# Performance work log

Hardware: AMD Instinct MI355X
Metric: run time of the kernel (lower is better)

Reference implementation:

```python
import jax, jax.numpy as jnp
import numpy as np

D_MODEL = 1024
N_HEADS = 16
D_K = D_MODEL // N_HEADS


def setup_inputs() -> dict:
    key = jax.random.key(0)
    ks = jax.random.split(key, 9)
    s = 1.0 / np.sqrt(D_MODEL)
    def lin(kw, kb):
        W = jax.random.uniform(kw, (D_MODEL, D_MODEL), jnp.float32, -s, s)
        b = jax.random.uniform(kb, (D_MODEL,), jnp.float32, -s, s)
        return W, b
    wq, bq = lin(ks[0], ks[1])
    wk, bk = lin(ks[2], ks[3])
    wv, bv = lin(ks[4], ks[5])
    wo, bo = lin(ks[6], ks[7])
    x = jax.random.normal(ks[8], (2, 2048, D_MODEL), jnp.float32)
    return {"x": x, "wq": wq, "bq": bq, "wk": wk, "bk": bk,
            "wv": wv, "bv": bv, "wo": wo, "bo": bo}


def reference(x, wq, bq, wk, bk, wv, bv, wo, bo):
    B, S, D = x.shape
    scale = 1.0 / np.sqrt(D_K)
    # projections (torch Linear: y = x W^T + b); W stored as [in,out] here
    q = x @ wq + bq
    k = x @ wk + bk
    v = x @ wv + bv
    # [B, H, S, d_k]
    q = q.reshape(B, S, N_HEADS, D_K).transpose(0, 2, 1, 3)
    k = k.reshape(B, S, N_HEADS, D_K).transpose(0, 2, 1, 3)
    v = v.reshape(B, S, N_HEADS, D_K).transpose(0, 2, 1, 3)
    scores = jnp.einsum('bhqd,bhkd->bhqk', q, k) * scale
    attn = jax.nn.softmax(scores, axis=-1)
    out = jnp.einsum('bhqk,bhkd->bhqd', attn, v)
    out = out.transpose(0, 2, 1, 3).reshape(B, S, D)
    return out @ wo + bo
```

## Files before the change

### kernel.cpp

```cpp
#include <hip/hip_runtime.h>
#include <hip/hip_bf16.h>
#include <math.h>

typedef __bf16 bf16x8 __attribute__((ext_vector_type(8)));
typedef unsigned short u16x8 __attribute__((ext_vector_type(8)));
typedef unsigned short u16x4 __attribute__((ext_vector_type(4)));
typedef float f32x4 __attribute__((ext_vector_type(4)));
typedef unsigned int u32x4 __attribute__((ext_vector_type(4)));
typedef unsigned int u32x2 __attribute__((ext_vector_type(2)));
typedef unsigned short u16;

__device__ __forceinline__ u16 f2bf(float f) {
    unsigned int x = __float_as_uint(f);
    x += 0x7fffu + ((x >> 16) & 1u);
    return (u16)(x >> 16);
}
__device__ __forceinline__ void glds16(const void* g, void* l) {
    __builtin_amdgcn_global_load_lds(
        (const __attribute__((address_space(1))) void*)g,
        (__attribute__((address_space(3))) void*)l, 16, 0, 0);
}
__device__ __forceinline__ void swap_half(unsigned& a, unsigned& b) {
    u32x2 t = __builtin_amdgcn_permlane32_swap(a, b, false, false);
    t = __builtin_amdgcn_permlane16_swap(t[0], t[1], false, false);
    a = t[0]; b = t[1];
}

__global__ __launch_bounds__(256) void prep(const float* __restrict__ W0, const float* __restrict__ W1,
                                            const float* __restrict__ W2, const float* __restrict__ W3,
                                            const float* __restrict__ X,
                                            u16* __restrict__ Wt, u16* __restrict__ Xb) {
    int z = blockIdx.z;
    if (z >= 4) {
        int row = (z - 4) * 1024 + blockIdx.y * 32 + blockIdx.x;
        const float* src = X + (size_t)row * 1024 + threadIdx.x * 4;
        f32x4 v = *(const f32x4*)src;
        u16x4 o; o[0] = f2bf(v[0]); o[1] = f2bf(v[1]); o[2] = f2bf(v[2]); o[3] = f2bf(v[3]);
        *(u16x4*)&Xb[(size_t)row * 1024 + threadIdx.x * 4] = o;
        return;
    }
    __shared__ float T[32][33];
    const float* W = (z == 0) ? W0 : ((z == 1) ? W1 : ((z == 2) ? W2 : W3));
    u16* dst = Wt + (size_t)z * 1024 * 1024;
    int k0 = blockIdx.y * 32, n0 = blockIdx.x * 32;
    int x = threadIdx.x & 31, y0 = threadIdx.x >> 5;
#pragma unroll
    for (int i = 0; i < 4; i++) {
        int y = y0 + i * 8;
        T[y][x] = W[(size_t)(k0 + y) * 1024 + n0 + x];
    }
    __syncthreads();
#pragma unroll
    for (int i = 0; i < 4; i++) {
        int y = y0 + i * 8;
        dst[(size_t)(n0 + y) * 1024 + k0 + x] = f2bf(T[x][y]);
    }
}

template <bool OF32, bool VSPLIT>
__global__ __launch_bounds__(256) void gemm(
    const u16* __restrict__ Bt,
    const float* __restrict__ b0, const float* __restrict__ b1, const float* __restrict__ b2,
    const u16* __restrict__ A, void* __restrict__ Cptr, u16* __restrict__ Vt, int Ntot)
{
    __shared__ __align__(16) u16 As[128 * 32];
    __shared__ __align__(16) u16 Bs[128 * 32];
    int tid = threadIdx.x;
    int lane = tid & 63, l15 = lane & 15, quad = lane >> 4;
    int wid = tid >> 6, wm = wid >> 1, wn = wid & 1;
    int m0 = blockIdx.y * 128, n0 = blockIdx.x * 128;
    int sel = n0 >> 10;
    const float* bias = (sel == 0) ? b0 : ((sel == 1) ? b1 : b2);

    f32x4 acc[4][4];
#pragma unroll
    for (int i = 0; i < 4; i++)
#pragma unroll
        for (int j = 0; j < 4; j++) { f32x4 z = {0.f, 0.f, 0.f, 0.f}; acc[i][j] = z; }

    int rr = lane >> 2;
    int cc = (lane & 3) ^ ((rr >> 1) & 3);
    const u16* abase = A  + (size_t)m0 * 1024;
    const u16* bbase = Bt + (size_t)n0 * 1024;
    int fsw = (l15 >> 1) & 3;

    for (int k0 = 0; k0 < 1024; k0 += 32) {
#pragma unroll
        for (int inst = 0; inst < 2; inst++) {
            int r0 = wid * 32 + inst * 16;
            glds16(&abase[(size_t)(r0 + rr) * 1024 + k0 + cc * 8], &As[r0 * 32]);
            glds16(&bbase[(size_t)(r0 + rr) * 1024 + k0 + cc * 8], &Bs[r0 * 32]);
        }
        __syncthreads();
        bf16x8 af[4], bf[4];
#pragma unroll
        for (int mt = 0; mt < 4; mt++)
            af[mt] = *(const bf16x8*)&As[(wm * 64 + mt * 16 + l15) * 32 + ((quad ^ fsw) * 8)];
#pragma unroll
        for (int nt = 0; nt < 4; nt++)
            bf[nt] = *(const bf16x8*)&Bs[(wn * 64 + nt * 16 + l15) * 32 + ((quad ^ fsw) * 8)];
#pragma unroll
        for (int mt = 0; mt < 4; mt++)
#pragma unroll
            for (int nt = 0; nt < 4; nt++)
                acc[mt][nt] = __builtin_amdgcn_mfma_f32_16x16x32_bf16(af[mt], bf[nt], acc[mt][nt], 0, 0, 0);
        __syncthreads();
    }
    if (VSPLIT && sel == 2) {
        int b = m0 >> 11;
#pragma unroll
        for (int mt = 0; mt < 4; mt++) {
            int gr = m0 + wm * 64 + mt * 16 + quad * 4;
            int s = gr & 2047;
#pragma unroll
            for (int nt = 0; nt < 4; nt++) {
                int gcl = (n0 & 1023) + wn * 64 + nt * 16 + l15;
                float bb = bias[gcl];
                u16x4 pk;
#pragma unroll
                for (int r = 0; r < 4; r++) pk[r] = f2bf(acc[mt][nt][r] + bb);
                *(u16x4*)&Vt[(size_t)((b * 16 + (gcl >> 6)) * 64 + (gcl & 63)) * 2048 + s] = pk;
            }
        }
        return;
    }
#pragma unroll
    for (int mt = 0; mt < 4; mt++) {
        int gr = m0 + wm * 64 + mt * 16 + quad * 4;
#pragma unroll
        for (int nt = 0; nt < 4; nt++) {
            int gc = n0 + wn * 64 + nt * 16 + l15;
            float bb = bias[gc & 1023];
#pragma unroll
            for (int r = 0; r < 4; r++) {
                float v = acc[mt][nt][r] + bb;
                if (OF32) ((float*)Cptr)[(size_t)(gr + r) * Ntot + gc] = v;
                else      ((u16*)Cptr)[(size_t)(gr + r) * Ntot + gc] = f2bf(v);
            }
        }
    }
}

__global__ __launch_bounds__(256) void attn(const u16* __restrict__ QKV,
                                            const u16* __restrict__ Vt,
                                            u16* __restrict__ O)
{
    __shared__ __align__(16) u16 Ks[2][64 * 64];
    __shared__ __align__(16) u16 Vs[2][64 * 64];
    const int S = 2048, DQ = 3072;
    int tid = threadIdx.x, wid = tid >> 6, lane = tid & 63;
    int l15 = lane & 15, quad = lane >> 4;
    int qt = blockIdx.x, h = blockIdx.y, b = blockIdx.z;
    const u16* base = QKV + (size_t)b * S * DQ + h * 64;
    const u16* Kb = base + 1024;
    const u16* Vtb = Vt + (size_t)((b * 16 + h) * 64) * 2048;
    int q0 = qt * 64 + wid * 16;

    bf16x8 qf0 = *(const bf16x8*)&base[(size_t)(q0 + l15) * DQ + quad * 8];
    bf16x8 qf1 = *(const bf16x8*)&base[(size_t)(q0 + l15) * DQ + 32 + quad * 8];

    f32x4 oacc[4];
#pragma unroll
    for (int i = 0; i < 4; i++) { f32x4 z = {0.f, 0.f, 0.f, 0.f}; oacc[i] = z; }
    float psum = 0.f;
    const float ls = 0.125f * 1.44269504088896f;

    int rr = lane >> 3;
    int cc = (lane & 7) ^ rr;
    int fs7 = l15 & 7;

    auto stage = [&](int it, int bsel) {
        int kv0 = it << 6;
#pragma unroll
        for (int inst = 0; inst < 2; inst++) {
            int r0 = wid * 16 + inst * 8;
            glds16(&Kb[(size_t)(kv0 + r0 + rr) * DQ + cc * 8], &Ks[bsel][r0 * 64]);
            glds16(&Vtb[(size_t)(r0 + rr) * 2048 + kv0 + cc * 8], &Vs[bsel][r0 * 64]);
        }
    };

    stage(0, 0);
#pragma unroll 2
    for (int it = 0; it < 32; ++it) {
        int cur = it & 1;
        if (it < 31) {
            stage(it + 1, cur ^ 1);
            asm volatile("s_waitcnt vmcnt(4)\n\ts_barrier" ::: "memory");
        } else {
            asm volatile("s_waitcnt vmcnt(0)\n\ts_barrier" ::: "memory");
        }

        f32x4 sa[4];
#pragma unroll
        for (int t = 0; t < 4; t++) { f32x4 z = {0.f, 0.f, 0.f, 0.f}; sa[t] = z; }
#pragma unroll
        for (int t = 0; t < 4; t++) {
            bf16x8 kfa = *(const bf16x8*)&Ks[cur][(t * 16 + l15) * 64 + ((quad ^ fs7) * 8)];
            bf16x8 kfb = *(const bf16x8*)&Ks[cur][(t * 16 + l15) * 64 + (((quad + 4) ^ fs7) * 8)];
            sa[t] = __builtin_amdgcn_mfma_f32_16x16x32_bf16(kfa, qf0, sa[t], 0, 0, 0);
            sa[t] = __builtin_amdgcn_mfma_f32_16x16x32_bf16(kfb, qf1, sa[t], 0, 0, 0);
        }

        unsigned wpk[4][2];
#pragma unroll
        for (int t = 0; t < 4; t++) {
            float e0 = __builtin_amdgcn_exp2f(sa[t][0] * ls);
            float e1 = __builtin_amdgcn_exp2f(sa[t][1] * ls);
            float e2 = __builtin_amdgcn_exp2f(sa[t][2] * ls);
            float e3 = __builtin_amdgcn_exp2f(sa[t][3] * ls);
            psum += (e0 + e1) + (e2 + e3);
            asm("v_cvt_pk_bf16_f32 %0, %1, %2" : "=v"(wpk[t][0]) : "v"(e0), "v"(e1));
            asm("v_cvt_pk_bf16_f32 %0, %1, %2" : "=v"(wpk[t][1]) : "v"(e2), "v"(e3));
        }
        unsigned a0 = wpk[0][0], a2 = wpk[1][0]; swap_half(a0, a2);
        unsigned a1 = wpk[0][1], a3 = wpk[1][1]; swap_half(a1, a3);
        unsigned c0 = wpk[2][0], c2 = wpk[3][0]; swap_half(c0, c2);
        unsigned c1 = wpk[2][1], c3 = wpk[3][1]; swap_half(c1, c3);
        u32x4 pd0 = {a0, a1, a2, a3};
        u32x4 pd1 = {c0, c1, c2, c3};
        bf16x8 pf0 = *(bf16x8*)&pd0;
        bf16x8 pf1 = *(bf16x8*)&pd1;

#pragma unroll
        for (int dt = 0; dt < 4; dt++) {
            bf16x8 vfa = *(const bf16x8*)&Vs[cur][(dt * 16 + l15) * 64 + ((quad ^ fs7) * 8)];
            bf16x8 vfb = *(const bf16x8*)&Vs[cur][(dt * 16 + l15) * 64 + (((quad + 4) ^ fs7) * 8)];
            oacc[dt] = __builtin_amdgcn_mfma_f32_16x16x32_bf16(pf0, vfa, oacc[dt], 0, 0, 0);
            oacc[dt] = __builtin_amdgcn_mfma_f32_16x16x32_bf16(pf1, vfb, oacc[dt], 0, 0, 0);
        }
        asm volatile("s_barrier" ::: "memory");
    }

    psum += __shfl_xor(psum, 16);
    psum += __shfl_xor(psum, 32);
#pragma unroll
    for (int r = 0; r < 4; r++) {
        float inv = 1.0f / __shfl(psum, quad * 4 + r);
        size_t row = (size_t)(b * S + q0 + quad * 4 + r);
#pragma unroll
        for (int dt = 0; dt < 4; dt++)
            O[row * 1024 + h * 64 + dt * 16 + l15] = f2bf(oacc[dt][r] * inv);
    }
}

extern "C" void kernel_launch(void* const* d_in, const int* in_sizes, int n_in,
                              void* d_out, int out_size, void* d_ws, size_t ws_size,
                              hipStream_t stream) {
    const float* x  = (const float*)d_in[0];
    const float* wq = (const float*)d_in[1];
    const float* bq = (const float*)d_in[2];
    const float* wk = (const float*)d_in[3];
    const float* bk = (const float*)d_in[4];
    const float* wv = (const float*)d_in[5];
    const float* bv = (const float*)d_in[6];
    const float* wo = (const float*)d_in[7];
    const float* bo = (const float*)d_in[8];
    float* out = (float*)d_out;

    u16* qkv  = (u16*)d_ws;
    u16* obuf = qkv  + (size_t)4096 * 3072;
    u16* vt   = obuf + (size_t)4096 * 1024;
    u16* wt   = vt   + (size_t)2048 * 2048;
    u16* xb   = wt   + (size_t)4 * 1024 * 1024;

    dim3 tb(256);
    prep<<<dim3(32, 32, 8), tb, 0, stream>>>(wq, wk, wv, wo, x, wt, xb);
    gemm<false, true><<<dim3(24, 32), tb, 0, stream>>>(wt, bq, bk, bv, xb, qkv, vt, 3072);
    attn<<<dim3(32, 16, 2), tb, 0, stream>>>(qkv, vt, obuf);
    gemm<true, false><<<dim3(8, 32), tb, 0, stream>>>(wt + (size_t)3 * 1024 * 1024,
                                                      bo, bo, bo, obuf, out, (u16*)nullptr, 1024);
}
```

Before: 210.1 us.

## Process 32 query rows per wave in attention and fold softmax scale into Q

Each attention wave now handles two 16-row query tiles, so every K and V fragment read from LDS feeds twice as many MFMAs. The grid is halved to match. The softmax scale and log2(e) factor move into the QKV GEMM epilogue for the Q slice, which removes one multiply per score. The cost is more registers per thread (launch bounds set to 2 blocks per SM) and half as many blocks to fill the GPU. The kernel still has no running-max subtraction, as before.

Measured after the change: 203.0 us. -3.4%, faster.

```diff
diff --git a/kernel.cpp b/kernel.cpp
--- a/kernel.cpp
+++ b/kernel.cpp
@@ -124,6 +124,7 @@
         }
         return;
     }
+    float qs = (VSPLIT && sel == 0) ? 0.18033688011112f : 1.0f;
 #pragma unroll
     for (int mt = 0; mt < 4; mt++) {
         int gr = m0 + wm * 64 + mt * 16 + quad * 4;
@@ -133,7 +134,7 @@
             float bb = bias[gc & 1023];
 #pragma unroll
             for (int r = 0; r < 4; r++) {
-                float v = acc[mt][nt][r] + bb;
+                float v = (acc[mt][nt][r] + bb) * qs;
                 if (OF32) ((float*)Cptr)[(size_t)(gr + r) * Ntot + gc] = v;
                 else      ((u16*)Cptr)[(size_t)(gr + r) * Ntot + gc] = f2bf(v);
             }
@@ -141,9 +142,9 @@
     }
 }
 
-__global__ __launch_bounds__(256) void attn(const u16* __restrict__ QKV,
-                                            const u16* __restrict__ Vt,
-                                            u16* __restrict__ O)
+__global__ __launch_bounds__(256, 2) void attn(const u16* __restrict__ QKV,
+                                               const u16* __restrict__ Vt,
+                                               u16* __restrict__ O)
 {
     __shared__ __align__(16) u16 Ks[2][64 * 64];
     __shared__ __align__(16) u16 Vs[2][64 * 64];
@@ -154,16 +155,17 @@
     const u16* base = QKV + (size_t)b * S * DQ + h * 64;
     const u16* Kb = base + 1024;
     const u16* Vtb = Vt + (size_t)((b * 16 + h) * 64) * 2048;
-    int q0 = qt * 64 + wid * 16;
-
-    bf16x8 qf0 = *(const bf16x8*)&base[(size_t)(q0 + l15) * DQ + quad * 8];
-    bf16x8 qf1 = *(const bf16x8*)&base[(size_t)(q0 + l15) * DQ + 32 + quad * 8];
-
-    f32x4 oacc[4];
-#pragma unroll
-    for (int i = 0; i < 4; i++) { f32x4 z = {0.f, 0.f, 0.f, 0.f}; oacc[i] = z; }
-    float psum = 0.f;
-    const float ls = 0.125f * 1.44269504088896f;
+    int q0 = qt * 128 + wid * 32;
+
+    bf16x8 qA0 = *(const bf16x8*)&base[(size_t)(q0 + l15) * DQ + quad * 8];
+    bf16x8 qA1 = *(const bf16x8*)&base[(size_t)(q0 + l15) * DQ + 32 + quad * 8];
+    bf16x8 qB0 = *(const bf16x8*)&base[(size_t)(q0 + 16 + l15) * DQ + quad * 8];
+    bf16x8 qB1 = *(const bf16x8*)&base[(size_t)(q0 + 16 + l15) * DQ + 32 + quad * 8];
+
+    f32x4 oA[4], oB[4];
+#pragma unroll
+    for (int i = 0; i < 4; i++) { f32x4 z = {0.f, 0.f, 0.f, 0.f}; oA[i] = z; oB[i] = z; }
+    float psA = 0.f, psB = 0.f;
 
     int rr = lane >> 3;
     int cc = (lane & 7) ^ rr;
@@ -190,56 +192,82 @@
             asm volatile("s_waitcnt vmcnt(0)\n\ts_barrier" ::: "memory");
         }
 
-        f32x4 sa[4];
-#pragma unroll
-        for (int t = 0; t < 4; t++) { f32x4 z = {0.f, 0.f, 0.f, 0.f}; sa[t] = z; }
+        f32x4 sA[4], sB[4];
+#pragma unroll
+        for (int t = 0; t < 4; t++) { f32x4 z = {0.f, 0.f, 0.f, 0.f}; sA[t] = z; sB[t] = z; }
 #pragma unroll
         for (int t = 0; t < 4; t++) {
             bf16x8 kfa = *(const bf16x8*)&Ks[cur][(t * 16 + l15) * 64 + ((quad ^ fs7) * 8)];
             bf16x8 kfb = *(const bf16x8*)&Ks[cur][(t * 16 + l15) * 64 + (((quad + 4) ^ fs7) * 8)];
-            sa[t] = __builtin_amdgcn_mfma_f32_16x16x32_bf16(kfa, qf0, sa[t], 0, 0, 0);
-            sa[t] = __builtin_amdgcn_mfma_f32_16x16x32_bf16(kfb, qf1, sa[t], 0, 0, 0);
-        }
-
-        unsigned wpk[4][2];
+            sA[t] = __builtin_amdgcn_mfma_f32_16x16x32_bf16(kfa, qA0, sA[t], 0, 0, 0);
+            sA[t] = __builtin_amdgcn_mfma_f32_16x16x32_bf16(kfb, qA1, sA[t], 0, 0, 0);
+            sB[t] = __builtin_amdgcn_mfma_f32_16x16x32_bf16(kfa, qB0, sB[t], 0, 0, 0);
+            sB[t] = __builtin_amdgcn_mfma_f32_16x16x32_bf16(kfb, qB1, sB[t], 0, 0, 0);
+        }
+
+        unsigned wA[4][2], wB[4][2];
 #pragma unroll
         for (int t = 0; t < 4; t++) {
-            float e0 = __builtin_amdgcn_exp2f(sa[t][0] * ls);
-            float e1 = __builtin_amdgcn_exp2f(sa[t][1] * ls);
-            float e2 = __builtin_amdgcn_exp2f(sa[t][2] * ls);
-            float e3 = __builtin_amdgcn_exp2f(sa[t][3] * ls);
-            psum += (e0 + e1) + (e2 + e3);
-            asm("v_cvt_pk_bf16_f32 %0, %1, %2" : "=v"(wpk[t][0]) : "v"(e0), "v"(e1));
-            asm("v_cvt_pk_bf16_f32 %0, %1, %2" : "=v"(wpk[t][1]) : "v"(e2), "v"(e3));
-        }
-        unsigned a0 = wpk[0][0], a2 = wpk[1][0]; swap_half(a0, a2);
-        unsigned a1 = wpk[0][1], a3 = wpk[1][1]; swap_half(a1, a3);
-        unsigned c0 = wpk[2][0], c2 = wpk[3][0]; swap_half(c0, c2);
-        unsigned c1 = wpk[2][1], c3 = wpk[3][1]; swap_half(c1, c3);
-        u32x4 pd0 = {a0, a1, a2, a3};
-        u32x4 pd1 = {c0, c1, c2, c3};
-        bf16x8 pf0 = *(bf16x8*)&pd0;
-        bf16x8 pf1 = *(bf16x8*)&pd1;
+            float a0 = __builtin_amdgcn_exp2f(sA[t][0]);
+            float a1 = __builtin_amdgcn_exp2f(sA[t][1]);
+            float a2 = __builtin_amdgcn_exp2f(sA[t][2]);
+            float a3 = __builtin_amdgcn_exp2f(sA[t][3]);
+            psA += (a0 + a1) + (a2 + a3);
+            asm("v_cvt_pk_bf16_f32 %0, %1, %2" : "=v"(wA[t][0]) : "v"(a0), "v"(a1));
+            asm("v_cvt_pk_bf16_f32 %0, %1, %2" : "=v"(wA[t][1]) : "v"(a2), "v"(a3));
+            float b0_ = __builtin_amdgcn_exp2f(sB[t][0]);
+            float b1_ = __builtin_amdgcn_exp2f(sB[t][1]);
+            float b2_ = __builtin_amdgcn_exp2f(sB[t][2]);
+            float b3_ = __builtin_amdgcn_exp2f(sB[t][3]);
+            psB += (b0_ + b1_) + (b2_ + b3_);
+            asm("v_cvt_pk_bf16_f32 %0, %1, %2" : "=v"(wB[t][0]) : "v"(b0_), "v"(b1_));
+            asm("v_cvt_pk_bf16_f32 %0, %1, %2" : "=v"(wB[t][1]) : "v"(b2_), "v"(b3_));
+        }
+        unsigned a0 = wA[0][0], a2 = wA[1][0]; swap_half(a0, a2);
+        unsigned a1 = wA[0][1], a3 = wA[1][1]; swap_half(a1, a3);
+        unsigned c0 = wA[2][0], c2 = wA[3][0]; swap_half(c0, c2);
+        unsigned c1 = wA[2][1], c3 = wA[3][1]; swap_half(c1, c3);
+        u32x4 pdA0 = {a0, a1, a2, a3};
+        u32x4 pdA1 = {c0, c1, c2, c3};
+        bf16x8 pfA0 = *(bf16x8*)&pdA0;
+        bf16x8 pfA1 = *(bf16x8*)&pdA1;
+        unsigned d0 = wB[0][0], d2 = wB[1][0]; swap_half(d0, d2);
+        unsigned d1 = wB[0][1], d3 = wB[1][1]; swap_half(d1, d3);
+        unsigned e0 = wB[2][0], e2 = wB[3][0]; swap_half(e0, e2);
+        unsigned e1 = wB[2][1], e3 = wB[3][1]; swap_half(e1, e3);
+        u32x4 pdB0 = {d0, d1, d2, d3};
+        u32x4 pdB1 = {e0, e1, e2, e3};
+        bf16x8 pfB0 = *(bf16x8*)&pdB0;
+        bf16x8 pfB1 = *(bf16x8*)&pdB1;
 
 #pragma unroll
         for (int dt = 0; dt < 4; dt++) {
             bf16x8 vfa = *(const bf16x8*)&Vs[cur][(dt * 16 + l15) * 64 + ((quad ^ fs7) * 8)];
             bf16x8 vfb = *(const bf16x8*)&Vs[cur][(dt * 16 + l15) * 64 + (((quad + 4) ^ fs7) * 8)];
-            oacc[dt] = __builtin_amdgcn_mfma_f32_16x16x32_bf16(pf0, vfa, oacc[dt], 0, 0, 0);
-            oacc[dt] = __builtin_amdgcn_mfma_f32_16x16x32_bf16(pf1, vfb, oacc[dt], 0, 0, 0);
+            oA[dt] = __builtin_amdgcn_mfma_f32_16x16x32_bf16(pfA0, vfa, oA[dt], 0, 0, 0);
+            oA[dt] = __builtin_amdgcn_mfma_f32_16x16x32_bf16(pfA1, vfb, oA[dt], 0, 0, 0);
+            oB[dt] = __builtin_amdgcn_mfma_f32_16x16x32_bf16(pfB0, vfa, oB[dt], 0, 0, 0);
+            oB[dt] = __builtin_amdgcn_mfma_f32_16x16x32_bf16(pfB1, vfb, oB[dt], 0, 0, 0);
         }
         asm volatile("s_barrier" ::: "memory");
     }
 
-    psum += __shfl_xor(psum, 16);
-    psum += __shfl_xor(psum, 32);
+    psA += __shfl_xor(psA, 16);
+    psA += __shfl_xor(psA, 32);
+    psB += __shfl_xor(psB, 16);
+    psB += __shfl_xor(psB, 32);
 #pragma unroll
     for (int r = 0; r < 4; r++) {
-        float inv = 1.0f / __shfl(psum, quad * 4 + r);
-        size_t row = (size_t)(b * S + q0 + quad * 4 + r);
+        float invA = 1.0f / __shfl(psA, quad * 4 + r);
+        size_t rowA = (size_t)(b * S + q0 + quad * 4 + r);
 #pragma unroll
         for (int dt = 0; dt < 4; dt++)
-            O[row * 1024 + h * 64 + dt * 16 + l15] = f2bf(oacc[dt][r] * inv);
+            O[rowA * 1024 + h * 64 + dt * 16 + l15] = f2bf(oA[dt][r] * invA);
+        float invB = 1.0f / __shfl(psB, quad * 4 + r);
+        size_t rowB = rowA + 16;
+#pragma unroll
+        for (int dt = 0; dt < 4; dt++)
+            O[rowB * 1024 + h * 64 + dt * 16 + l15] = f2bf(oB[dt][r] * invB);
     }
 }
 
@@ -266,7 +294,7 @@
     dim3 tb(256);
     prep<<<dim3(32, 32, 8), tb, 0, stream>>>(wq, wk, wv, wo, x, wt, xb);
     gemm<false, true><<<dim3(24, 32), tb, 0, stream>>>(wt, bq, bk, bv, xb, qkv, vt, 3072);
-    attn<<<dim3(32, 16, 2), tb, 0, stream>>>(qkv, vt, obuf);
+    attn<<<dim3(16, 16, 2), tb, 0, stream>>>(qkv, vt, obuf);
     gemm<true, false><<<dim3(8, 32), tb, 0, stream>>>(wt + (size_t)3 * 1024 * 1024,
                                                       bo, bo, bo, obuf, out, (u16*)nullptr, 1024);
 }
```
